# Kernel optimization log

Hardware: AMD Instinct MI355X
Metric: run time of the kernel (lower is better)

The kernel has to match this reference:

```python
import jax, jax.numpy as jnp
import numpy as np

NUM_LAYERS = 2
MAG = 5 / 10.0  # magnitude=5 on a 0-10 scale
FILL = 0.5      # gray fill for out-of-bounds pixels (images in [0,1])
ENH = 1.0 + 0.9 * MAG  # enhancement factor magnitude (brightness/contrast/sharpness)


def _bilinear(img, xi, yi):
    H, W, _ = img.shape
    x0 = jnp.floor(xi); y0 = jnp.floor(yi)
    wx = xi - x0; wy = yi - y0
    def gather(yy, xx):
        valid = (xx >= 0) & (xx <= W - 1) & (yy >= 0) & (yy <= H - 1)
        v = img[jnp.clip(yy, 0, H - 1).astype(jnp.int32),
                jnp.clip(xx, 0, W - 1).astype(jnp.int32)]
        return jnp.where(valid[..., None], v, FILL)
    return (gather(y0, x0) * ((1 - wx) * (1 - wy))[..., None]
            + gather(y0, x0 + 1) * (wx * (1 - wy))[..., None]
            + gather(y0 + 1, x0) * ((1 - wx) * wy)[..., None]
            + gather(y0 + 1, x0 + 1) * (wx * wy)[..., None])


def _affine(img, a, b, tx, c, d, ty):
    # inverse affine map about image center, bilinear resample
    H, W, _ = img.shape
    ys, xs = jnp.meshgrid(jnp.arange(H, dtype=jnp.float32),
                          jnp.arange(W, dtype=jnp.float32), indexing='ij')
    cx = (W - 1) * 0.5; cy = (H - 1) * 0.5
    xi = a * (xs - cx) + b * (ys - cy) + tx + cx
    yi = c * (xs - cx) + d * (ys - cy) + ty + cy
    return _bilinear(img, xi, yi)


def _blend(a, b, f):
    return jnp.clip(a + f * (b - a), 0.0, 1.0)


def _smooth(img):
    # 3x3 smoothing kernel used by PIL/TF sharpness
    k = jnp.array([[1., 1., 1.], [1., 5., 1.], [1., 1., 1.]], jnp.float32) / 13.0
    H, W, _ = img.shape
    p = jnp.pad(img, ((1, 1), (1, 1), (0, 0)), mode='edge')
    out = jnp.zeros_like(img)
    for i in range(3):
        for j in range(3):
            out = out + k[i, j] * p[i:i + H, j:j + W]
    return out


def _rotate(img, s):
    th = s * (30.0 * MAG) * (np.pi / 180.0)
    co, si = jnp.cos(th), jnp.sin(th)
    return _affine(img, co, si, 0.0, -si, co, 0.0)

def _shear_x(img, s):
    sh = s * 0.3 * MAG
    return _affine(img, 1.0, -sh, 0.0, 0.0, 1.0, 0.0)

def _shear_y(img, s):
    sh = s * 0.3 * MAG
    return _affine(img, 1.0, 0.0, 0.0, -sh, 1.0, 0.0)

def _trans_x(img, s):
    t = s * 0.3 * MAG * img.shape[1]
    return _affine(img, 1.0, 0.0, -t, 0.0, 1.0, 0.0)

def _trans_y(img, s):
    t = s * 0.3 * MAG * img.shape[0]
    return _affine(img, 1.0, 0.0, 0.0, 0.0, 1.0, -t)

def _brightness(img, s):
    f = jnp.where(s > 0, ENH, 1.0 / ENH)
    return _blend(jnp.zeros_like(img), img, f)

def _contrast(img, s):
    f = jnp.where(s > 0, ENH, 1.0 / ENH)
    return _blend(jnp.mean(img) * jnp.ones_like(img), img, f)

def _sharpness(img, s):
    f = jnp.where(s > 0, ENH, 1.0 / ENH)
    return _blend(_smooth(img), img, f)


BRANCHES = [_rotate, _shear_x, _shear_y, _trans_x, _trans_y,
            _brightness, _contrast, _sharpness]


def _apply_one(img, ops, signs):
    # img: [H,W,3]; ops, signs: [NUM_LAYERS]
    for l in range(NUM_LAYERS):
        s = (2 * signs[l] - 1).astype(jnp.float32)
        img = jax.lax.switch(ops[l], BRANCHES, img, s)
    return img


def setup_inputs() -> dict:
    key = jax.random.key(0)
    k1, k2, k3 = jax.random.split(key, 3)
    B, H, W = 64, 512, 512
    images = jax.random.uniform(k1, (B, H, W, 3), dtype=jnp.float32)
    op_ids = jax.random.randint(k2, (B, NUM_LAYERS), 0, len(BRANCHES), dtype=jnp.int32)
    signs = jax.random.randint(k3, (B, NUM_LAYERS), 0, 2, dtype=jnp.int32)
    return {"images": images, "op_ids": op_ids, "signs": signs}


def reference(images, op_ids, signs):
    return jax.vmap(_apply_one)(images, op_ids, signs)
```

## Files before the change

### kernel.cpp

```cpp
#include <hip/hip_runtime.h>
#include <math.h>

#define IMH 512
#define IMW 512
#define NIMG 64
#define NPIX (IMH*IMW)
#define NELEM (NPIX*3)
#define CXF 255.5f
#define CYF 255.5f
#define ENHF 1.45f
#define INVENHF (1.0f/1.45f)
#define FILLF 0.5f
#define MBPI0 64
#define TW 32
#define TH 32
#define MAXLDS 1700

struct F3 { float x, y, z; };

__device__ __forceinline__ F3 mk3(float v){ F3 r; r.x=v; r.y=v; r.z=v; return r; }

__device__ __forceinline__ F3 ldpix(const float* __restrict__ im, int y, int x){
  const float* p = im + (y*IMW + x)*3;
  F3 r; r.x=p[0]; r.y=p[1]; r.z=p[2]; return r;
}

__device__ __forceinline__ F3 clip01(F3 v){
  F3 r;
  r.x = fminf(fmaxf(v.x, 0.f), 1.f);
  r.y = fminf(fmaxf(v.y, 0.f), 1.f);
  r.z = fminf(fmaxf(v.z, 0.f), 1.f);
  return r;
}

__device__ __forceinline__ void affine_params(int op, float s,
    float& a, float& b, float& tx, float& c, float& d, float& ty){
  a = 1.f; b = 0.f; tx = 0.f; c = 0.f; d = 1.f; ty = 0.f;
  if (op == 0){
    a = 0.96592582628907f; b = s * 0.25881904510252f; c = -b; d = a;
  } else if (op == 1){
    b = -s * 0.15f;
  } else if (op == 2){
    c = -s * 0.15f;
  } else if (op == 3){
    tx = -s * 76.8f;
  } else if (op == 4){
    ty = -s * 76.8f;
  }
}

__device__ __forceinline__ F3 bilin_interior(const float* __restrict__ im, float xi, float yi){
  float x0f = floorf(xi), y0f = floorf(yi);
  float wx = xi - x0f, wy = yi - y0f;
  float w00=(1.f-wx)*(1.f-wy), w01=wx*(1.f-wy), w10=(1.f-wx)*wy, w11=wx*wy;
  const float* p0 = im + ((int)y0f*IMW + (int)x0f)*3;
  const float* p1 = p0 + IMW*3;
  F3 r;
  r.x = w00*p0[0]+w01*p0[3]+w10*p1[0]+w11*p1[3];
  r.y = w00*p0[1]+w01*p0[4]+w10*p1[1]+w11*p1[4];
  r.z = w00*p0[2]+w01*p0[5]+w10*p1[2]+w11*p1[5];
  return r;
}

__device__ __forceinline__ F3 bilin_img(const float* __restrict__ im, float xi, float yi){
  float x0f = floorf(xi), y0f = floorf(yi);
  float wx = xi - x0f, wy = yi - y0f;
  int x0 = (int)x0f, y0 = (int)y0f;
  F3 r;
  if (x0 >= 0 && y0 >= 0 && x0 < IMW-1 && y0 < IMH-1){
    return bilin_interior(im, xi, yi);
  }
  r = mk3(0.f);
  #pragma unroll
  for (int cidx = 0; cidx < 4; cidx++){
    int dx = cidx & 1, dy = cidx >> 1;
    int xx = x0 + dx, yy = y0 + dy;
    float w = (dx ? wx : (1.f - wx)) * (dy ? wy : (1.f - wy));
    F3 v;
    if (xx >= 0 && xx < IMW && yy >= 0 && yy < IMH)
      v = ldpix(im, yy, xx);
    else
      v = mk3(FILLF);
    r.x += w * v.x; r.y += w * v.y; r.z += w * v.z;
  }
  return r;
}

__device__ F3 eval0(const float* __restrict__ im, int op, float s, float mean0, int x, int y){
  if (op < 5){
    float a,b,tx,c,d,ty; affine_params(op, s, a, b, tx, c, d, ty);
    float fx = (float)x - CXF, fy = (float)y - CYF;
    return bilin_img(im, a*fx + b*fy + tx + CXF, c*fx + d*fy + ty + CYF);
  }
  F3 v = ldpix(im, y, x);
  float f = (s > 0.f) ? ENHF : INVENHF;
  if (op == 5){
    F3 r; r.x = f*v.x; r.y = f*v.y; r.z = f*v.z; return clip01(r);
  }
  if (op == 6){
    F3 r;
    r.x = mean0 + f*(v.x - mean0);
    r.y = mean0 + f*(v.y - mean0);
    r.z = mean0 + f*(v.z - mean0);
    return clip01(r);
  }
  F3 sm; sm.x = (5.f/13.f)*v.x; sm.y = (5.f/13.f)*v.y; sm.z = (5.f/13.f)*v.z;
  #pragma unroll
  for (int dy = -1; dy <= 1; dy++){
    #pragma unroll
    for (int dx = -1; dx <= 1; dx++){
      if (dx == 0 && dy == 0) continue;
      int yy = min(max(y + dy, 0), IMH-1);
      int xx = min(max(x + dx, 0), IMW-1);
      F3 q = ldpix(im, yy, xx);
      sm.x += (1.f/13.f)*q.x; sm.y += (1.f/13.f)*q.y; sm.z += (1.f/13.f)*q.z;
    }
  }
  F3 r;
  r.x = sm.x + f*(v.x - sm.x);
  r.y = sm.y + f*(v.y - sm.y);
  r.z = sm.z + f*(v.z - sm.z);
  return clip01(r);
}

__device__ __forceinline__ float block_reduce(float v){
  #pragma unroll
  for (int off = 32; off > 0; off >>= 1) v += __shfl_down(v, off, 64);
  __shared__ float sm[4];
  int lane = threadIdx.x & 63, wid = threadIdx.x >> 6;
  if (lane == 0) sm[wid] = v;
  __syncthreads();
  float r = 0.f;
  if (threadIdx.x == 0) r = sm[0] + sm[1] + sm[2] + sm[3];
  return r;
}

__global__ __launch_bounds__(256) void mean0_kernel(const float* __restrict__ images,
    const int* __restrict__ ops, float* __restrict__ means){
  int img = blockIdx.x / MBPI0;
  if (ops[2*img] != 6) return;
  const float4* im = (const float4*)(images + (size_t)img * NELEM);
  float s = 0.f;
  for (int i = (blockIdx.x % MBPI0)*256 + threadIdx.x; i < NELEM/4; i += MBPI0*256){
    float4 v = im[i];
    s += v.x + v.y + v.z + v.w;
  }
  s = block_reduce(s);
  if (threadIdx.x == 0) atomicAdd(&means[2*img], s * (1.0f/(float)NELEM));
}

__device__ __forceinline__ void store4(float* __restrict__ out, int img, int y, int xbase,
                                       const F3* res){
  float4 o0 = make_float4(res[0].x, res[0].y, res[0].z, res[1].x);
  float4 o1 = make_float4(res[1].y, res[1].z, res[2].x, res[2].y);
  float4 o2 = make_float4(res[2].z, res[3].x, res[3].y, res[3].z);
  float4* op = (float4*)(out + ((size_t)img * NPIX + (size_t)y * IMW + xbase) * 3);
  op[0] = o0; op[1] = o1; op[2] = o2;
}

__global__ __launch_bounds__(256, 8) void apply_kernel(const float* __restrict__ images,
    const int* __restrict__ ops, const int* __restrict__ signs,
    float* __restrict__ means, float* __restrict__ out){
  int img  = blockIdx.x >> 8;
  int tile = blockIdx.x & 255;
  int tx0 = (tile & 15) * TW;
  int ty0 = (tile >> 4) * TH;
  const float* im = images + (size_t)img * NELEM;
  int op0 = ops[2*img], op1 = ops[2*img + 1];
  float s0 = signs[2*img]     ? 1.f : -1.f;
  float s1 = signs[2*img + 1] ? 1.f : -1.f;
  float mean0 = means[2*img];

  int row   = threadIdx.x >> 3;
  int xbase = tx0 + ((threadIdx.x & 7) << 2);
  int y     = ty0 + row;
  float f1 = (s1 > 0.f) ? ENHF : INVENHF;

  if (op1 == 5 || op1 == 6){
    F3 v4[4];
    if (op0 < 5){
      float a0,b0,t0x,c0,d0,t0y; affine_params(op0, s0, a0,b0,t0x,c0,d0,t0y);
      float fxl = (float)tx0 - CXF, fxr = (float)(tx0+TW-1) - CXF;
      float fyt = (float)ty0 - CYF, fyb = (float)(ty0+TH-1) - CYF;
      float xA = a0*fxl + b0*fyt, xB = a0*fxr + b0*fyt, xC = a0*fxl + b0*fyb, xD = a0*fxr + b0*fyb;
      float yA = c0*fxl + d0*fyt, yB = c0*fxr + d0*fyt, yC = c0*fxl + d0*fyb, yD = c0*fxr + d0*fyb;
      float sxmin = fminf(fminf(xA,xB),fminf(xC,xD)) + t0x + CXF;
      float sxmax = fmaxf(fmaxf(xA,xB),fmaxf(xC,xD)) + t0x + CXF;
      float symin = fminf(fminf(yA,yB),fminf(yC,yD)) + t0y + CYF;
      float symax = fmaxf(fmaxf(yA,yB),fmaxf(yC,yD)) + t0y + CYF;
      bool inter = (sxmin >= 1.f) && (symin >= 1.f) &&
                   (sxmax <= (float)(IMW-2)) && (symax <= (float)(IMH-2));
      float fy = (float)y - CYF;
      if (inter){
        #pragma unroll
        for (int q = 0; q < 4; q++){
          float fx = (float)(xbase + q) - CXF;
          v4[q] = bilin_interior(im, a0*fx + b0*fy + t0x + CXF, c0*fx + d0*fy + t0y + CYF);
        }
      } else {
        #pragma unroll
        for (int q = 0; q < 4; q++){
          float fx = (float)(xbase + q) - CXF;
          v4[q] = bilin_img(im, a0*fx + b0*fy + t0x + CXF, c0*fx + d0*fy + t0y + CYF);
        }
      }
    } else {
      #pragma unroll
      for (int q = 0; q < 4; q++)
        v4[q] = eval0(im, op0, s0, mean0, xbase + q, y);
    }
    F3 res[4];
    float ssum = 0.f;
    #pragma unroll
    for (int q = 0; q < 4; q++){
      if (op1 == 5){
        F3 o; o.x = f1*v4[q].x; o.y = f1*v4[q].y; o.z = f1*v4[q].z;
        res[q] = clip01(o);
      } else {
        res[q] = v4[q];
        ssum += v4[q].x + v4[q].y + v4[q].z;
      }
    }
    store4(out, img, y, xbase, res);
    if (op1 == 6){
      ssum = block_reduce(ssum);
      if (threadIdx.x == 0) atomicAdd(&means[2*img + 1], ssum * (1.0f/(float)NELEM));
    }
    return;
  }

  float a1=1.f,b1=0.f,txx=0.f,c1=0.f,d1=1.f,tyy=0.f;
  int pbx0, pby0, pbx1, pby1;
  if (op1 < 5){
    affine_params(op1, s1, a1, b1, txx, c1, d1, tyy);
    float xmin = 1e30f, xmax = -1e30f, ymin = 1e30f, ymax = -1e30f;
    #pragma unroll
    for (int i = 0; i < 4; i++){
      float fx = (float)(tx0 + (i & 1) * (TW - 1)) - CXF;
      float fy = (float)(ty0 + (i >> 1) * (TH - 1)) - CYF;
      float xi = a1*fx + b1*fy + txx + CXF;
      float yi = c1*fx + d1*fy + tyy + CYF;
      xmin = fminf(xmin, xi); xmax = fmaxf(xmax, xi);
      ymin = fminf(ymin, yi); ymax = fmaxf(ymax, yi);
    }
    pbx0 = (int)floorf(xmin); pbx1 = (int)floorf(xmax) + 1;
    pby0 = (int)floorf(ymin); pby1 = (int)floorf(ymax) + 1;
  } else {
    pbx0 = tx0 - 1; pbx1 = tx0 + TW; pby0 = ty0 - 1; pby1 = ty0 + TH;
  }
  int bx0 = max(pbx0, 0), by0 = max(pby0, 0);
  int bx1 = min(pbx1, IMW - 1), by1 = min(pby1, IMH - 1);
  int bw = bx1 - bx0 + 1, bh = by1 - by0 + 1;
  int nstage = (bw > 0 && bh > 0) ? bw * bh : 0;
  bool l1_interior = (op1 < 5) && pbx0 >= 0 && pby0 >= 0 && pbx1 <= IMW-1 && pby1 <= IMH-1;

  __shared__ float lds[MAXLDS * 3];
  if (nstage > 0){
    int Kq = 256 / bw, Rr = 256 - Kq * bw;
    int iy = (int)threadIdx.x / bw;
    int ix = (int)threadIdx.x - iy * bw;
    if (op0 < 5){
      float a0,b0,t0x,c0,d0,t0y; affine_params(op0, s0, a0,b0,t0x,c0,d0,t0y);
      float Cx = a0*((float)bx0 - CXF) + b0*((float)by0 - CYF) + t0x + CXF;
      float Cy = c0*((float)bx0 - CXF) + d0*((float)by0 - CYF) + t0y + CYF;
      float w = (float)(bw - 1), h = (float)(bh - 1);
      float x00 = Cx, x10 = Cx + a0*w, x01 = Cx + b0*h, x11 = Cx + a0*w + b0*h;
      float y00 = Cy, y10 = Cy + c0*w, y01 = Cy + d0*h, y11 = Cy + c0*w + d0*h;
      float sxmin = fminf(fminf(x00,x10),fminf(x01,x11));
      float sxmax = fmaxf(fmaxf(x00,x10),fmaxf(x01,x11));
      float symin = fminf(fminf(y00,y10),fminf(y01,y11));
      float symax = fmaxf(fmaxf(y00,y10),fmaxf(y01,y11));
      bool inter = (sxmin >= 1.f) && (symin >= 1.f) &&
                   (sxmax <= (float)(IMW-2)) && (symax <= (float)(IMH-2));
      if (inter){
        int idx = threadIdx.x;
        float cwx = 0.f, cwy = 0.f;
        const float* cp0 = im;
        float A0=0,A1=0,A2=0,A3=0,A4=0,A5=0,B0=0,B1=0,B2=0,B3=0,B4=0,B5=0;
        if (idx < nstage){
          float xi = a0*(float)ix + b0*(float)iy + Cx;
          float yi = c0*(float)ix + d0*(float)iy + Cy;
          float x0f = floorf(xi), y0f = floorf(yi);
          cwx = xi - x0f; cwy = yi - y0f;
          cp0 = im + ((int)y0f*IMW + (int)x0f)*3;
          A0=cp0[0];A1=cp0[1];A2=cp0[2];A3=cp0[3];A4=cp0[4];A5=cp0[5];
          const float* cp1 = cp0 + IMW*3;
          B0=cp1[0];B1=cp1[1];B2=cp1[2];B3=cp1[3];B4=cp1[4];B5=cp1[5];
        }
        while (idx < nstage){
          int nidx = idx + 256;
          int nix = ix + Rr, niy = iy + Kq;
          if (nix >= bw){ nix -= bw; niy += 1; }
          float nwx = 0.f, nwy = 0.f;
          float NA0=0,NA1=0,NA2=0,NA3=0,NA4=0,NA5=0,NB0=0,NB1=0,NB2=0,NB3=0,NB4=0,NB5=0;
          if (nidx < nstage){
            float xi = a0*(float)nix + b0*(float)niy + Cx;
            float yi = c0*(float)nix + d0*(float)niy + Cy;
            float x0f = floorf(xi), y0f = floorf(yi);
            nwx = xi - x0f; nwy = yi - y0f;
            const float* np0 = im + ((int)y0f*IMW + (int)x0f)*3;
            NA0=np0[0];NA1=np0[1];NA2=np0[2];NA3=np0[3];NA4=np0[4];NA5=np0[5];
            const float* np1 = np0 + IMW*3;
            NB0=np1[0];NB1=np1[1];NB2=np1[2];NB3=np1[3];NB4=np1[4];NB5=np1[5];
          }
          float w00=(1.f-cwx)*(1.f-cwy), w01=cwx*(1.f-cwy), w10=(1.f-cwx)*cwy, w11=cwx*cwy;
          lds[idx*3+0] = w00*A0 + w01*A3 + w10*B0 + w11*B3;
          lds[idx*3+1] = w00*A1 + w01*A4 + w10*B1 + w11*B4;
          lds[idx*3+2] = w00*A2 + w01*A5 + w10*B2 + w11*B5;
          idx = nidx; ix = nix; iy = niy; cwx = nwx; cwy = nwy;
          A0=NA0;A1=NA1;A2=NA2;A3=NA3;A4=NA4;A5=NA5;
          B0=NB0;B1=NB1;B2=NB2;B3=NB3;B4=NB4;B5=NB5;
        }
      } else {
        for (int idx = threadIdx.x; idx < nstage; idx += 256){
          float xi = a0*(float)ix + b0*(float)iy + Cx;
          float yi = c0*(float)ix + d0*(float)iy + Cy;
          F3 v = bilin_img(im, xi, yi);
          lds[idx*3+0]=v.x; lds[idx*3+1]=v.y; lds[idx*3+2]=v.z;
          ix += Rr; iy += Kq; if (ix >= bw){ ix -= bw; iy += 1; }
        }
      }
    } else {
      for (int idx = threadIdx.x; idx < nstage; idx += 256){
        F3 v = eval0(im, op0, s0, mean0, bx0 + ix, by0 + iy);
        lds[idx*3+0]=v.x; lds[idx*3+1]=v.y; lds[idx*3+2]=v.z;
        ix += Rr; iy += Kq; if (ix >= bw){ ix -= bw; iy += 1; }
      }
    }
  }
  __syncthreads();

  F3 res[4];
  if (op1 < 5 && l1_interior){
    float fy = (float)y - CYF;
    #pragma unroll
    for (int q = 0; q < 4; q++){
      float fx = (float)(xbase + q) - CXF;
      float xi = a1*fx + b1*fy + txx + CXF;
      float yi = c1*fx + d1*fy + tyy + CYF;
      float x0f = fminf(fmaxf(floorf(xi), (float)bx0), (float)(bx1-1));
      float y0f = fminf(fmaxf(floorf(yi), (float)by0), (float)(by1-1));
      float wx = xi - x0f, wy = yi - y0f;
      float w00=(1.f-wx)*(1.f-wy), w01=wx*(1.f-wy), w10=(1.f-wx)*wy, w11=wx*wy;
      const float* q0 = lds + (((int)y0f - by0) * bw + ((int)x0f - bx0)) * 3;
      const float* q1 = q0 + bw * 3;
      F3 o;
      o.x = w00*q0[0] + w01*q0[3] + w10*q1[0] + w11*q1[3];
      o.y = w00*q0[1] + w01*q0[4] + w10*q1[1] + w11*q1[4];
      o.z = w00*q0[2] + w01*q0[5] + w10*q1[2] + w11*q1[5];
      res[q] = clip01(o);
    }
  } else {
    #pragma unroll
    for (int q = 0; q < 4; q++){
      int x = xbase + q;
      F3 o;
      if (op1 < 5){
        float fx = (float)x - CXF, fy = (float)y - CYF;
        float xi = a1*fx + b1*fy + txx + CXF;
        float yi = c1*fx + d1*fy + tyy + CYF;
        float xf0 = floorf(xi), yf0 = floorf(yi);
        float wx = xi - xf0, wy = yi - yf0;
        int x0 = (int)xf0, y0 = (int)yf0;
        o = mk3(0.f);
        #pragma unroll
        for (int ci = 0; ci < 4; ci++){
          int dx = ci & 1, dy = ci >> 1;
          int xx = x0 + dx, yy = y0 + dy;
          float wq = (dx ? wx : (1.f - wx)) * (dy ? wy : (1.f - wy));
          F3 v;
          if (xx >= 0 && xx < IMW && yy >= 0 && yy < IMH){
            int lx = min(max(xx - bx0, 0), bw - 1);
            int ly = min(max(yy - by0, 0), bh - 1);
            int li = (ly * bw + lx) * 3;
            v.x = lds[li]; v.y = lds[li+1]; v.z = lds[li+2];
          } else v = mk3(FILLF);
          o.x += wq * v.x; o.y += wq * v.y; o.z += wq * v.z;
        }
      } else {
        int li0 = ((y - by0) * bw + (x - bx0)) * 3;
        F3 v; v.x = lds[li0]; v.y = lds[li0+1]; v.z = lds[li0+2];
        F3 sm; sm.x = (5.f/13.f)*v.x; sm.y = (5.f/13.f)*v.y; sm.z = (5.f/13.f)*v.z;
        #pragma unroll
        for (int dy = -1; dy <= 1; dy++){
          #pragma unroll
          for (int dx = -1; dx <= 1; dx++){
            if (dx == 0 && dy == 0) continue;
            int yy = min(max(y + dy, 0), IMH-1);
            int xx = min(max(x + dx, 0), IMW-1);
            int li = ((yy - by0) * bw + (xx - bx0)) * 3;
            sm.x += (1.f/13.f)*lds[li];
            sm.y += (1.f/13.f)*lds[li+1];
            sm.z += (1.f/13.f)*lds[li+2];
          }
        }
        o.x = sm.x + f1*(v.x - sm.x);
        o.y = sm.y + f1*(v.y - sm.y);
        o.z = sm.z + f1*(v.z - sm.z);
      }
      res[q] = clip01(o);
    }
  }

  store4(out, img, y, xbase, res);
}

__global__ __launch_bounds__(256) void fixup_kernel(const int* __restrict__ ops,
    const int* __restrict__ signs, const float* __restrict__ means,
    float* __restrict__ out){
  int img = blockIdx.x >> 8;
  if (ops[2*img + 1] != 6) return;
  float f = signs[2*img + 1] ? ENHF : INVENHF;
  float m = means[2*img + 1];
  float4* p = (float4*)(out + (size_t)img * NELEM);
  const int n = NELEM / 4;
  for (int i = (blockIdx.x & 255)*256 + threadIdx.x; i < n; i += 256*256){
    float4 v = p[i];
    v.x = fminf(fmaxf(m + f*(v.x - m), 0.f), 1.f);
    v.y = fminf(fmaxf(m + f*(v.y - m), 0.f), 1.f);
    v.z = fminf(fmaxf(m + f*(v.z - m), 0.f), 1.f);
    v.w = fminf(fmaxf(m + f*(v.w - m), 0.f), 1.f);
    p[i] = v;
  }
}

extern "C" void kernel_launch(void* const* d_in, const int* in_sizes, int n_in,
                              void* d_out, int out_size, void* d_ws, size_t ws_size,
                              hipStream_t stream){
  const float* images = (const float*)d_in[0];
  const int*   ops    = (const int*)d_in[1];
  const int*   signs  = (const int*)d_in[2];
  float* out   = (float*)d_out;
  float* means = (float*)d_ws;

  hipMemsetAsync(means, 0, 2*NIMG*sizeof(float), stream);
  mean0_kernel<<<NIMG*MBPI0, 256, 0, stream>>>(images, ops, means);
  apply_kernel<<<NIMG*256, 256, 0, stream>>>(images, ops, signs, means, out);
  fixup_kernel<<<NIMG*256, 256, 0, stream>>>(ops, signs, means, out);
}
```

Baseline: 401.3 us.

## Add direct path for pointwise op0 followed by affine op1, interleave image blocks

Adds a fast path for the case where the first op is brightness or contrast and the second is an affine warp. It applies the pointwise op inline to each bilinear tap read from global memory, instead of going through the general LDS staging path. It also remaps block indices so consecutive blocks cover different images, which changes scheduling and cache locality. Applying the pointwise op per tap recomputes it up to four times per pixel, but avoids staging.

```diff
diff --git a/kernel.cpp b/kernel.cpp
--- a/kernel.cpp
+++ b/kernel.cpp
@@ -33,6 +33,11 @@
   return r;
 }
 
+__device__ __forceinline__ float gpw(float v, int op0, float f0, float m0){
+  float r = (op0 == 5) ? f0*v : m0 + f0*(v - m0);
+  return fminf(fmaxf(r, 0.f), 1.f);
+}
+
 __device__ __forceinline__ void affine_params(int op, float s,
     float& a, float& b, float& tx, float& c, float& d, float& ty){
   a = 1.f; b = 0.f; tx = 0.f; c = 0.f; d = 1.f; ty = 0.f;
@@ -86,6 +91,40 @@
   return r;
 }
 
+__device__ __forceinline__ F3 bilin_gpw(const float* __restrict__ im, float xi, float yi,
+                                        int op0, float f0, float m0){
+  float x0f = floorf(xi), y0f = floorf(yi);
+  float wx = xi - x0f, wy = yi - y0f;
+  int x0 = (int)x0f, y0 = (int)y0f;
+  F3 r;
+  if (x0 >= 0 && y0 >= 0 && x0 < IMW-1 && y0 < IMH-1){
+    float w00=(1.f-wx)*(1.f-wy), w01=wx*(1.f-wy), w10=(1.f-wx)*wy, w11=wx*wy;
+    const float* p0 = im + (y0*IMW + x0)*3;
+    const float* p1 = p0 + IMW*3;
+    r.x = w00*gpw(p0[0],op0,f0,m0) + w01*gpw(p0[3],op0,f0,m0)
+        + w10*gpw(p1[0],op0,f0,m0) + w11*gpw(p1[3],op0,f0,m0);
+    r.y = w00*gpw(p0[1],op0,f0,m0) + w01*gpw(p0[4],op0,f0,m0)
+        + w10*gpw(p1[1],op0,f0,m0) + w11*gpw(p1[4],op0,f0,m0);
+    r.z = w00*gpw(p0[2],op0,f0,m0) + w01*gpw(p0[5],op0,f0,m0)
+        + w10*gpw(p1[2],op0,f0,m0) + w11*gpw(p1[5],op0,f0,m0);
+    return r;
+  }
+  r = mk3(0.f);
+  #pragma unroll
+  for (int cidx = 0; cidx < 4; cidx++){
+    int dx = cidx & 1, dy = cidx >> 1;
+    int xx = x0 + dx, yy = y0 + dy;
+    float w = (dx ? wx : (1.f - wx)) * (dy ? wy : (1.f - wy));
+    F3 v;
+    if (xx >= 0 && xx < IMW && yy >= 0 && yy < IMH){
+      F3 q = ldpix(im, yy, xx);
+      v.x = gpw(q.x,op0,f0,m0); v.y = gpw(q.y,op0,f0,m0); v.z = gpw(q.z,op0,f0,m0);
+    } else v = mk3(FILLF);
+    r.x += w * v.x; r.y += w * v.y; r.z += w * v.z;
+  }
+  return r;
+}
+
 __device__ F3 eval0(const float* __restrict__ im, int op, float s, float mean0, int x, int y){
   if (op < 5){
     float a,b,tx,c,d,ty; affine_params(op, s, a, b, tx, c, d, ty);
@@ -161,8 +200,8 @@
 __global__ __launch_bounds__(256, 8) void apply_kernel(const float* __restrict__ images,
     const int* __restrict__ ops, const int* __restrict__ signs,
     float* __restrict__ means, float* __restrict__ out){
-  int img  = blockIdx.x >> 8;
-  int tile = blockIdx.x & 255;
+  int img  = blockIdx.x & 63;
+  int tile = blockIdx.x >> 6;
   int tx0 = (tile & 15) * TW;
   int ty0 = (tile >> 4) * TH;
   const float* im = images + (size_t)img * NELEM;
@@ -170,6 +209,7 @@
   float s0 = signs[2*img]     ? 1.f : -1.f;
   float s1 = signs[2*img + 1] ? 1.f : -1.f;
   float mean0 = means[2*img];
+  float f0 = (s0 > 0.f) ? ENHF : INVENHF;
 
   int row   = threadIdx.x >> 3;
   int xbase = tx0 + ((threadIdx.x & 7) << 2);
@@ -226,6 +266,21 @@
       ssum = block_reduce(ssum);
       if (threadIdx.x == 0) atomicAdd(&means[2*img + 1], ssum * (1.0f/(float)NELEM));
     }
+    return;
+  }
+
+  if (op1 < 5 && (op0 == 5 || op0 == 6)){
+    float a1,b1,txx,c1,d1,tyy; affine_params(op1, s1, a1,b1,txx,c1,d1,tyy);
+    float fy = (float)y - CYF;
+    F3 res[4];
+    #pragma unroll
+    for (int q = 0; q < 4; q++){
+      float fx = (float)(xbase + q) - CXF;
+      float xi = a1*fx + b1*fy + txx + CXF;
+      float yi = c1*fx + d1*fy + tyy + CYF;
+      res[q] = clip01(bilin_gpw(im, xi, yi, op0, f0, mean0));
+    }
+    store4(out, img, y, xbase, res);
     return;
   }
 
@@ -275,14 +330,13 @@
       if (inter){
         int idx = threadIdx.x;
         float cwx = 0.f, cwy = 0.f;
-        const float* cp0 = im;
         float A0=0,A1=0,A2=0,A3=0,A4=0,A5=0,B0=0,B1=0,B2=0,B3=0,B4=0,B5=0;
         if (idx < nstage){
           float xi = a0*(float)ix + b0*(float)iy + Cx;
           float yi = c0*(float)ix + d0*(float)iy + Cy;
           float x0f = floorf(xi), y0f = floorf(yi);
           cwx = xi - x0f; cwy = yi - y0f;
-          cp0 = im + ((int)y0f*IMW + (int)x0f)*3;
+          const float* cp0 = im + ((int)y0f*IMW + (int)x0f)*3;
           A0=cp0[0];A1=cp0[1];A2=cp0[2];A3=cp0[3];A4=cp0[4];A5=cp0[5];
           const float* cp1 = cp0 + IMW*3;
           B0=cp1[0];B1=cp1[1];B2=cp1[2];B3=cp1[3];B4=cp1[4];B5=cp1[5];
```

Result: slower. 458.7 us (+14.3%).
